# Kernel tuning notes

Hardware: AMD Instinct MI355X
Metric: run time of the kernel (lower is better)

The kernel has to match this reference:

```python
import jax, jax.numpy as jnp
import numpy as np

N_NODES = 50000
N_EDGES = 800000
IN_F, HID_F, OUT_F = 512, 128, 16


def setup_inputs() -> dict:
    key = jax.random.key(0)
    k1, k2, k3, k4, k5, k6 = jax.random.split(key, 6)
    x = jax.random.normal(k1, (N_NODES, IN_F), dtype=jnp.float32)
    edge_src = jax.random.randint(k2, (N_EDGES,), 0, N_NODES, dtype=jnp.int32)
    edge_dst = jax.random.randint(k3, (N_EDGES,), 0, N_NODES, dtype=jnp.int32)
    edge_val = jax.random.uniform(k4, (N_EDGES,), dtype=jnp.float32)
    # Xavier uniform init like torch.nn.init.xavier_uniform_
    lim1 = float(np.sqrt(6.0 / (IN_F + HID_F)))
    lim2 = float(np.sqrt(6.0 / (HID_F + OUT_F)))
    W1 = jax.random.uniform(k5, (IN_F, HID_F), minval=-lim1, maxval=lim1, dtype=jnp.float32)
    W2 = jax.random.uniform(k6, (HID_F, OUT_F), minval=-lim2, maxval=lim2, dtype=jnp.float32)
    return {"x": x, "edge_src": edge_src, "edge_dst": edge_dst, "edge_val": edge_val, "W1": W1, "W2": W2}


def _spmm(edge_val, edge_src, edge_dst, dense, n_nodes):
    # out[i] = sum_{e: dst(e)=i} val(e) * dense[src(e)]  == sparse_adj @ dense
    gathered = edge_val[:, None] * dense[edge_src]  # [E, F]
    return jax.ops.segment_sum(gathered, edge_dst, num_segments=n_nodes)


def reference(x, edge_src, edge_dst, edge_val, W1, W2):
    n = x.shape[0]
    # layer 1: mm -> spmm -> relu
    h = jax.nn.relu(_spmm(edge_val, edge_src, edge_dst, x @ W1, n))
    # dropout(p=0.5) is identity in eval mode (training=False)
    # layer 2: mm -> spmm (no relu)
    logits = _spmm(edge_val, edge_src, edge_dst, h @ W2, n)
    return jax.nn.log_softmax(logits, axis=1)
```

## Files before the change

### kernel.cpp

```cpp
#include <hip/hip_runtime.h>
#include <hip/hip_fp16.h>

#define N_NODES 50000
#define N_EDGES 800000
#define IN_F    512
#define HID_F   128
#define OUT_F   16
#define CAP     64
#define GEMM_BLOCKS 1563
#define FILL_BLOCKS 782
#define FAT_BLOCKS  2346

typedef __attribute__((ext_vector_type(8))) short short8v;
typedef __attribute__((ext_vector_type(4))) float float4v;
typedef unsigned int uint32;
typedef unsigned short ushort16;

typedef __attribute__((address_space(3))) void lds_vp;
typedef __attribute__((address_space(1))) const void g_vp;

__device__ __forceinline__ ushort16 f2bf(float f) {
    uint32 u = __float_as_uint(f);
    uint32 r = (u + 0x7FFFu + ((u >> 16) & 1u)) >> 16;
    return (ushort16)r;
}
__device__ __forceinline__ float bf_lo(uint32 h) { return __uint_as_float(h << 16); }
__device__ __forceinline__ float bf_hi(uint32 h) { return __uint_as_float(h & 0xFFFF0000u); }
__device__ __forceinline__ uint32 pack2bf(float a, float b) {
    return (uint32)f2bf(a) | ((uint32)f2bf(b) << 16);
}
__device__ __forceinline__ float pk_val(uint32 u) {
    return __half2float(__ushort_as_half((unsigned short)(u >> 16)));
}

__global__ __launch_bounds__(256) void prep(const float* __restrict__ W1,
                                            unsigned short* __restrict__ W1T,
                                            int* __restrict__ cursor) {
    const int idx = blockIdx.x * 256 + threadIdx.x;
    if (idx < IN_F * HID_F) {
        const int k = idx >> 7;
        const int c = idx & 127;
        W1T[(size_t)c * IN_F + k] = (unsigned short)f2bf(W1[idx]);
    }
    if (idx < N_NODES) cursor[idx] = 0;
}

__global__ __launch_bounds__(256) void fill_and_gemm1(
        const int* __restrict__ src, const int* __restrict__ dst,
        const float* __restrict__ val, int* __restrict__ cursor,
        uint32* __restrict__ bucket,
        const float* __restrict__ X, const short* __restrict__ W1T,
        ushort16* __restrict__ H0) {
    __shared__ float4  Xs[512];
    __shared__ short8v Ws[1024];
    if ((blockIdx.x % 3) == 2) {
        const int fb = blockIdx.x / 3;
        const int e0 = fb * 1024 + threadIdx.x;
        int  dd[4], ss[4];
        float vv[4];
        bool ok[4];
#pragma unroll
        for (int q = 0; q < 4; ++q) {
            const int e = e0 + q * 256;
            ok[q] = (e < N_EDGES);
            if (ok[q]) { dd[q] = dst[e]; ss[q] = src[e]; vv[q] = val[e]; }
        }
        int pp[4];
#pragma unroll
        for (int q = 0; q < 4; ++q)
            if (ok[q]) pp[q] = atomicAdd(&cursor[dd[q]], 1);
#pragma unroll
        for (int q = 0; q < 4; ++q) {
            if (ok[q] && pp[q] < CAP) {
                const unsigned short hb = __half_as_ushort(__float2half_rn(vv[q]));
                bucket[(size_t)dd[q] * CAP + pp[q]] = (uint32)ss[q] | ((uint32)hb << 16);
            }
        }
        return;
    }
    const int gid = (blockIdx.x / 3) * 2 + (blockIdx.x % 3);
    if (gid >= GEMM_BLOCKS) return;
    const int t    = threadIdx.x;
    const int lane = t & 63;
    const int w    = t >> 6;
    const int wr   = w >> 1;
    const int wc   = w & 1;
    const int l15  = lane & 15;
    const int kg   = (lane >> 4) * 8;
    const int bm   = gid * 32;

    float4v acc[4];
#pragma unroll
    for (int n = 0; n < 4; ++n) acc[n] = (float4v){0.f, 0.f, 0.f, 0.f};

    const int ra = wr * 16 + l15;

    for (int k0 = 0; k0 < IN_F; k0 += 64) {
#pragma unroll
        for (int i = 0; i < 2; ++i) {
            const int idx = i * 256 + t;
            const int r   = idx >> 4;
            const int s   = idx & 15;
            const int c4  = s ^ (r & 15);
            const int grow = min(bm + r, N_NODES - 1);
            const float* g = X + (size_t)grow * IN_F + k0 + c4 * 4;
            __builtin_amdgcn_global_load_lds((g_vp*)g, (lds_vp*)&Xs[idx], 16, 0, 0);
        }
#pragma unroll
        for (int i = 0; i < 4; ++i) {
            const int idx = i * 256 + t;
            const int col = idx >> 3;
            const int s   = idx & 7;
            const int gsl = s ^ (col & 7);
            const short* g = W1T + (size_t)col * IN_F + k0 + gsl * 8;
            __builtin_amdgcn_global_load_lds((g_vp*)g, (lds_vp*)&Ws[idx], 16, 0, 0);
        }
        __syncthreads();
#pragma unroll
        for (int ks = 0; ks < 64; ks += 32) {
            const int j0 = (ks + kg) >> 2;
            const float4 a0 = Xs[ra * 16 + ((j0)     ^ (ra & 15))];
            const float4 a1 = Xs[ra * 16 + ((j0 + 1) ^ (ra & 15))];
            short8v af;
            af[0] = (short)f2bf(a0.x); af[1] = (short)f2bf(a0.y);
            af[2] = (short)f2bf(a0.z); af[3] = (short)f2bf(a0.w);
            af[4] = (short)f2bf(a1.x); af[5] = (short)f2bf(a1.y);
            af[6] = (short)f2bf(a1.z); af[7] = (short)f2bf(a1.w);
            const int gbn = (ks + kg) >> 3;
#pragma unroll
            for (int n = 0; n < 4; ++n) {
                const int col = wc * 64 + n * 16 + l15;
                const short8v bf = Ws[col * 8 + (gbn ^ (col & 7))];
                acc[n] = __builtin_amdgcn_mfma_f32_16x16x32_bf16(af, bf, acc[n], 0, 0, 0);
            }
        }
        __syncthreads();
    }

    const int crow0 = bm + wr * 16 + (lane >> 4) * 4;
#pragma unroll
    for (int rr = 0; rr < 4; ++rr) {
        const int grow = crow0 + rr;
        if (grow < N_NODES) {
#pragma unroll
            for (int n = 0; n < 4; ++n)
                H0[(size_t)grow * HID_F + wc * 64 + n * 16 + l15] = f2bf(acc[n][rr]);
        }
    }
}

__global__ __launch_bounds__(256) void spmm1_bucket(const uint32* __restrict__ H0u,
                                                    const int* __restrict__ cursor,
                                                    const uint32* __restrict__ bucket,
                                                    uint32* __restrict__ S1) {
    const int r    = blockIdx.x * 4 + (threadIdx.x >> 6);
    const int lane = threadIdx.x & 63;
    if (r >= N_NODES) return;
    const int cnt = min(cursor[r], CAP);
    const uint32 pk = bucket[(size_t)r * CAP + lane];
    float a0 = 0.f, a1 = 0.f;
    int j = 0;
    for (; j + 16 <= cnt; j += 16) {
        uint32 uu[16], hh[16];
#pragma unroll
        for (int q = 0; q < 16; ++q) {
            uu[q] = __shfl(pk, j + q);
            hh[q] = H0u[(size_t)(uu[q] & 0xFFFF) * 64 + lane];
        }
#pragma unroll
        for (int q = 0; q < 16; ++q) {
            const float v = pk_val(uu[q]);
            a0 += v * bf_lo(hh[q]);
            a1 += v * bf_hi(hh[q]);
        }
    }
    for (; j + 8 <= cnt; j += 8) {
        uint32 uu[8], hh[8];
#pragma unroll
        for (int q = 0; q < 8; ++q) {
            uu[q] = __shfl(pk, j + q);
            hh[q] = H0u[(size_t)(uu[q] & 0xFFFF) * 64 + lane];
        }
#pragma unroll
        for (int q = 0; q < 8; ++q) {
            const float v = pk_val(uu[q]);
            a0 += v * bf_lo(hh[q]);
            a1 += v * bf_hi(hh[q]);
        }
    }
    for (; j < cnt; ++j) {
        const uint32 u = __shfl(pk, j);
        const uint32 h = H0u[(size_t)(u & 0xFFFF) * 64 + lane];
        const float v  = pk_val(u);
        a0 += v * bf_lo(h);
        a1 += v * bf_hi(h);
    }
    S1[(size_t)r * 64 + lane] = pack2bf(fmaxf(a0, 0.f), fmaxf(a1, 0.f));
}

__global__ __launch_bounds__(256) void gemm2(const uint32* __restrict__ S1,
                                             const float* __restrict__ W2,
                                             float* __restrict__ H2) {
    __shared__ float w[HID_F * OUT_F];
    const int t = threadIdx.x;
#pragma unroll
    for (int i = 0; i < 8; ++i) w[t + i * 256] = W2[t + i * 256];
    __syncthreads();
    const int c    = t & 15;
    const int rloc = t >> 4;
    const int r    = blockIdx.x * 16 + rloc;
    if (r >= N_NODES) return;
    const uint32* row = S1 + (size_t)r * 64;
    float acc = 0.f;
#pragma unroll 8
    for (int k2 = 0; k2 < 64; ++k2) {
        const uint32 h = row[k2];
        acc += bf_lo(h) * w[(2 * k2) * OUT_F + c];
        acc += bf_hi(h) * w[(2 * k2 + 1) * OUT_F + c];
    }
    H2[(size_t)r * OUT_F + c] = acc;
}

__global__ __launch_bounds__(256) void spmm2_ls(const float* __restrict__ H2,
                                                const int* __restrict__ cursor,
                                                const uint32* __restrict__ bucket,
                                                float* __restrict__ out) {
    const int r = blockIdx.x * 16 + (threadIdx.x >> 4);
    const int f = threadIdx.x & 15;
    if (r >= N_NODES) return;
    const int cnt = min(cursor[r], CAP);
    float acc = 0.f;
    for (int base = 0; base < cnt; base += 16) {
        const uint32 pk = bucket[(size_t)r * CAP + base + f];
        const int lim = min(16, cnt - base);
        int j = 0;
        for (; j + 8 <= lim; j += 8) {
            uint32 uu[8];
            float  hh[8];
#pragma unroll
            for (int q = 0; q < 8; ++q) {
                uu[q] = __shfl(pk, j + q, 16);
                hh[q] = H2[(size_t)(uu[q] & 0xFFFF) * OUT_F + f];
            }
#pragma unroll
            for (int q = 0; q < 8; ++q) acc += pk_val(uu[q]) * hh[q];
        }
        for (; j < lim; ++j) {
            const uint32 u = __shfl(pk, j, 16);
            acc += pk_val(u) * H2[(size_t)(u & 0xFFFF) * OUT_F + f];
        }
    }
    float m = acc;
#pragma unroll
    for (int off = 1; off < 16; off <<= 1) m = fmaxf(m, __shfl_xor(m, off, 16));
    const float ex = __expf(acc - m);
    float ss = ex;
#pragma unroll
    for (int off = 1; off < 16; off <<= 1) ss += __shfl_xor(ss, off, 16);
    out[(size_t)r * OUT_F + f] = acc - m - logf(ss);
}

extern "C" void kernel_launch(void* const* d_in, const int* in_sizes, int n_in,
                              void* d_out, int out_size, void* d_ws, size_t ws_size,
                              hipStream_t stream) {
    const float* x        = (const float*)d_in[0];
    const int*   edge_src = (const int*)d_in[1];
    const int*   edge_dst = (const int*)d_in[2];
    const float* edge_val = (const float*)d_in[3];
    const float* W1       = (const float*)d_in[4];
    const float* W2       = (const float*)d_in[5];
    float* out = (float*)d_out;

    char* ws = (char*)d_ws;
    size_t off = 0;
    ushort16* H0  = (ushort16*)(ws + off); off += (size_t)N_NODES * HID_F * 2;
    uint32* S1    = (uint32*)  (ws + off); off += (size_t)N_NODES * HID_F * 2;
    uint32* bucket= (uint32*)  (ws + off); off += (size_t)N_NODES * CAP * 4;
    int*   cursor = (int*)     (ws + off); off += (size_t)N_NODES * 4;
    unsigned short* W1T = (unsigned short*)(ws + off); off += (size_t)IN_F * HID_F * 2;
    float* H2 = (float*)H0;

    prep<<<(IN_F * HID_F + 255) / 256, 256, 0, stream>>>(W1, W1T, cursor);

    fill_and_gemm1<<<FAT_BLOCKS, 256, 0, stream>>>(edge_src, edge_dst, edge_val,
                                                   cursor, bucket,
                                                   x, (const short*)W1T, H0);

    spmm1_bucket<<<(N_NODES + 3) / 4, 256, 0, stream>>>((const uint32*)H0, cursor, bucket, S1);

    gemm2<<<(N_NODES + 15) / 16, 256, 0, stream>>>(S1, W2, H2);

    spmm2_ls<<<(N_NODES + 15) / 16, 256, 0, stream>>>(H2, cursor, bucket, out);
}
```

Before: 117.1 us.

## Fuse second GEMM into first SpMM and enlarge GEMM1 row tile

The hidden-layer SpMM kernel now applies ReLU and multiplies its row by W2 in registers, reducing across the wavefront with shuffles, so the separate gemm2 kernel and the S1 intermediate round trip disappear. GEMM1 tiles grow from 32 to 64 rows per block, with each wave owning 16 rows and all 128 columns, and fill blocks now interleave one-to-one with GEMM blocks. The fused epilogue adds 16 six-step shuffle reductions per row, and the larger GEMM tile uses more LDS and accumulator registers, which can lower occupancy.

```diff
diff --git a/kernel.cpp b/kernel.cpp
--- a/kernel.cpp
+++ b/kernel.cpp
@@ -7,9 +7,8 @@
 #define HID_F   128
 #define OUT_F   16
 #define CAP     64
-#define GEMM_BLOCKS 1563
-#define FILL_BLOCKS 782
-#define FAT_BLOCKS  2346
+#define GEMM_BLOCKS 782
+#define FAT_BLOCKS  1564
 
 typedef __attribute__((ext_vector_type(8))) short short8v;
 typedef __attribute__((ext_vector_type(4))) float float4v;
@@ -26,9 +25,6 @@
 }
 __device__ __forceinline__ float bf_lo(uint32 h) { return __uint_as_float(h << 16); }
 __device__ __forceinline__ float bf_hi(uint32 h) { return __uint_as_float(h & 0xFFFF0000u); }
-__device__ __forceinline__ uint32 pack2bf(float a, float b) {
-    return (uint32)f2bf(a) | ((uint32)f2bf(b) << 16);
-}
 __device__ __forceinline__ float pk_val(uint32 u) {
     return __half2float(__ushort_as_half((unsigned short)(u >> 16)));
 }
@@ -51,10 +47,10 @@
         uint32* __restrict__ bucket,
         const float* __restrict__ X, const short* __restrict__ W1T,
         ushort16* __restrict__ H0) {
-    __shared__ float4  Xs[512];
+    __shared__ float4  Xs[1024];
     __shared__ short8v Ws[1024];
-    if ((blockIdx.x % 3) == 2) {
-        const int fb = blockIdx.x / 3;
+    if (blockIdx.x & 1) {
+        const int fb = blockIdx.x >> 1;
         const int e0 = fb * 1024 + threadIdx.x;
         int  dd[4], ss[4];
         float vv[4];
@@ -78,26 +74,23 @@
         }
         return;
     }
-    const int gid = (blockIdx.x / 3) * 2 + (blockIdx.x % 3);
-    if (gid >= GEMM_BLOCKS) return;
+    const int gid  = blockIdx.x >> 1;
     const int t    = threadIdx.x;
     const int lane = t & 63;
     const int w    = t >> 6;
-    const int wr   = w >> 1;
-    const int wc   = w & 1;
     const int l15  = lane & 15;
     const int kg   = (lane >> 4) * 8;
-    const int bm   = gid * 32;
-
-    float4v acc[4];
-#pragma unroll
-    for (int n = 0; n < 4; ++n) acc[n] = (float4v){0.f, 0.f, 0.f, 0.f};
-
-    const int ra = wr * 16 + l15;
+    const int bm   = gid * 64;
+
+    float4v acc[8];
+#pragma unroll
+    for (int n = 0; n < 8; ++n) acc[n] = (float4v){0.f, 0.f, 0.f, 0.f};
+
+    const int ra = w * 16 + l15;
 
     for (int k0 = 0; k0 < IN_F; k0 += 64) {
 #pragma unroll
-        for (int i = 0; i < 2; ++i) {
+        for (int i = 0; i < 4; ++i) {
             const int idx = i * 256 + t;
             const int r   = idx >> 4;
             const int s   = idx & 15;
@@ -128,8 +121,8 @@
             af[6] = (short)f2bf(a1.z); af[7] = (short)f2bf(a1.w);
             const int gbn = (ks + kg) >> 3;
 #pragma unroll
-            for (int n = 0; n < 4; ++n) {
-                const int col = wc * 64 + n * 16 + l15;
+            for (int n = 0; n < 8; ++n) {
+                const int col = n * 16 + l15;
                 const short8v bf = Ws[col * 8 + (gbn ^ (col & 7))];
                 acc[n] = __builtin_amdgcn_mfma_f32_16x16x32_bf16(af, bf, acc[n], 0, 0, 0);
             }
@@ -137,24 +130,31 @@
         __syncthreads();
     }
 
-    const int crow0 = bm + wr * 16 + (lane >> 4) * 4;
+    const int crow0 = bm + w * 16 + (lane >> 4) * 4;
 #pragma unroll
     for (int rr = 0; rr < 4; ++rr) {
         const int grow = crow0 + rr;
         if (grow < N_NODES) {
 #pragma unroll
-            for (int n = 0; n < 4; ++n)
-                H0[(size_t)grow * HID_F + wc * 64 + n * 16 + l15] = f2bf(acc[n][rr]);
-        }
-    }
-}
-
-__global__ __launch_bounds__(256) void spmm1_bucket(const uint32* __restrict__ H0u,
-                                                    const int* __restrict__ cursor,
-                                                    const uint32* __restrict__ bucket,
-                                                    uint32* __restrict__ S1) {
-    const int r    = blockIdx.x * 4 + (threadIdx.x >> 6);
-    const int lane = threadIdx.x & 63;
+            for (int n = 0; n < 8; ++n)
+                H0[(size_t)grow * HID_F + n * 16 + l15] = f2bf(acc[n][rr]);
+        }
+    }
+}
+
+__global__ __launch_bounds__(256) void spmm1_g2(const uint32* __restrict__ H0u,
+                                                const int* __restrict__ cursor,
+                                                const uint32* __restrict__ bucket,
+                                                const float* __restrict__ W2,
+                                                float* __restrict__ H2) {
+    __shared__ float w2s[HID_F * OUT_F];
+    const int t = threadIdx.x;
+#pragma unroll
+    for (int i = 0; i < 8; ++i) w2s[t + i * 256] = W2[t + i * 256];
+    __syncthreads();
+
+    const int r    = blockIdx.x * 4 + (t >> 6);
+    const int lane = t & 63;
     if (r >= N_NODES) return;
     const int cnt = min(cursor[r], CAP);
     const uint32 pk = bucket[(size_t)r * CAP + lane];
@@ -195,30 +195,20 @@
         a0 += v * bf_lo(h);
         a1 += v * bf_hi(h);
     }
-    S1[(size_t)r * 64 + lane] = pack2bf(fmaxf(a0, 0.f), fmaxf(a1, 0.f));
-}
-
-__global__ __launch_bounds__(256) void gemm2(const uint32* __restrict__ S1,
-                                             const float* __restrict__ W2,
-                                             float* __restrict__ H2) {
-    __shared__ float w[HID_F * OUT_F];
-    const int t = threadIdx.x;
-#pragma unroll
-    for (int i = 0; i < 8; ++i) w[t + i * 256] = W2[t + i * 256];
-    __syncthreads();
-    const int c    = t & 15;
-    const int rloc = t >> 4;
-    const int r    = blockIdx.x * 16 + rloc;
-    if (r >= N_NODES) return;
-    const uint32* row = S1 + (size_t)r * 64;
-    float acc = 0.f;
-#pragma unroll 8
-    for (int k2 = 0; k2 < 64; ++k2) {
-        const uint32 h = row[k2];
-        acc += bf_lo(h) * w[(2 * k2) * OUT_F + c];
-        acc += bf_hi(h) * w[(2 * k2 + 1) * OUT_F + c];
-    }
-    H2[(size_t)r * OUT_F + c] = acc;
+    a0 = fmaxf(a0, 0.f);
+    a1 = fmaxf(a1, 0.f);
+    float part[OUT_F];
+#pragma unroll
+    for (int c = 0; c < OUT_F; ++c)
+        part[c] = a0 * w2s[(2 * lane) * OUT_F + c] + a1 * w2s[(2 * lane + 1) * OUT_F + c];
+#pragma unroll
+    for (int off = 32; off > 0; off >>= 1)
+#pragma unroll
+        for (int c = 0; c < OUT_F; ++c)
+            part[c] += __shfl_xor(part[c], off);
+#pragma unroll
+    for (int c = 0; c < OUT_F; ++c)
+        if (lane == c) H2[(size_t)r * OUT_F + c] = part[c];
 }
 
 __global__ __launch_bounds__(256) void spmm2_ls(const float* __restrict__ H2,
@@ -274,11 +264,10 @@
     char* ws = (char*)d_ws;
     size_t off = 0;
     ushort16* H0  = (ushort16*)(ws + off); off += (size_t)N_NODES * HID_F * 2;
-    uint32* S1    = (uint32*)  (ws + off); off += (size_t)N_NODES * HID_F * 2;
+    float* H2     = (float*)   (ws + off); off += (size_t)N_NODES * OUT_F * 4;
     uint32* bucket= (uint32*)  (ws + off); off += (size_t)N_NODES * CAP * 4;
     int*   cursor = (int*)     (ws + off); off += (size_t)N_NODES * 4;
     unsigned short* W1T = (unsigned short*)(ws + off); off += (size_t)IN_F * HID_F * 2;
-    float* H2 = (float*)H0;
 
     prep<<<(IN_F * HID_F + 255) / 256, 256, 0, stream>>>(W1, W1T, cursor);
 
@@ -286,9 +275,7 @@
                                                    cursor, bucket,
                                                    x, (const short*)W1T, H0);
 
-    spmm1_bucket<<<(N_NODES + 3) / 4, 256, 0, stream>>>((const uint32*)H0, cursor, bucket, S1);
-
-    gemm2<<<(N_NODES + 15) / 16, 256, 0, stream>>>(S1, W2, H2);
+    spmm1_g2<<<(N_NODES + 3) / 4, 256, 0, stream>>>((const uint32*)H0, cursor, bucket, W2, H2);
 
     spmm2_ls<<<(N_NODES + 15) / 16, 256, 0, stream>>>(H2, cursor, bucket, out);
 }
```

Result: slower. 154.4 us (+31.8%).
